# Kernel optimization log

Hardware: AMD Instinct MI355X
Metric: run time of the kernel (lower is better)

Reference implementation:

```python
import jax, jax.numpy as jnp
import numpy as np

WINDOW = 32
MALIS_LR = 1.0
MALIS_LR_POS = 1.0


def _make_node_indexes(w):
    idx = np.arange(w * w).reshape(w, w)
    h = np.stack([idx[:, :-1].ravel(), idx[:, 1:].ravel()])
    v = np.stack([idx[:-1, :].ravel(), idx[1:, :].ravel()])
    return np.concatenate([h, v], axis=1)  # [2, 2*w*(w-1)]


class _UF:
    def __init__(self, n):
        self.p = list(range(n))

    def find(self, x):
        p = self.p
        while p[x] != x:
            p[x] = p[p[x]]
            x = p[x]
        return x


def _label8(mask):
    """skimage.measure.label with full (8-)connectivity: labels>=1 inside mask, 0 outside."""
    h, w = mask.shape
    n = h * w
    uf = _UF(n)
    idx = np.arange(n).reshape(h, w)
    pairs = []
    for (a, b) in (
        (idx[:, :-1], idx[:, 1:]),      # right
        (idx[:-1, :], idx[1:, :]),      # down
        (idx[:-1, :-1], idx[1:, 1:]),   # down-right
        (idx[:-1, 1:], idx[1:, :-1]),   # down-left
    ):
        m = mask.ravel()[a.ravel()] & mask.ravel()[b.ravel()]
        pairs.append(np.stack([a.ravel()[m], b.ravel()[m]], 1))
    for a, b in np.concatenate(pairs, 0):
        ra, rb = uf.find(int(a)), uf.find(int(b))
        if ra != rb:
            uf.p[rb] = ra
    labels = np.zeros(n, dtype=np.int64)
    root_lab = {}
    nxt = 1
    flat = mask.ravel()
    for i in range(n):
        if flat[i]:
            r = uf.find(i)
            if r not in root_lab:
                root_lab[r] = nxt
                nxt += 1
            labels[i] = root_lab[r]
    return labels


def _malis_weights(seg, n1, n2, costs, pos):
    """MALIS pair counts per edge: Kruskal maximin over edges in descending cost order;
    nodes with seg label 0 (foreground in this loss) carry no labels and contribute no pairs."""
    n = seg.shape[0]
    uf = _UF(n)
    overlap = [({int(seg[i]): 1} if seg[i] != 0 else {}) for i in range(n)]
    w = np.zeros(costs.shape[0], dtype=np.int64)
    order = np.argsort(-costs, kind="stable")
    for e in order:
        ra, rb = uf.find(int(n1[e])), uf.find(int(n2[e]))
        if ra == rb:
            continue
        oa, ob = overlap[ra], overlap[rb]
        tot_a = sum(oa.values())
        npair = 0
        for l2, c2 in ob.items():
            same = oa.get(l2, 0)
            npair += c2 * (same if pos else (tot_a - same))
        w[int(e)] = npair
        uf.p[rb] = ra
        for l2, c2 in ob.items():
            oa[l2] = oa.get(l2, 0) + c2
        overlap[rb] = {}
    return w


def _connectivity_weights(y_true_np, y_pred_np, window):
    B, C, H, W = y_pred_np.shape
    ni = _make_node_indexes(window)
    n1, n2 = ni[0], ni[1]
    weights_n = np.zeros_like(y_pred_np, dtype=np.float64)
    weights_p = np.zeros_like(y_pred_np, dtype=np.float64)
    half = window * (window - 1)
    for r in range(H // window):
        for c in range(W // window):
            rs = slice(r * window, (r + 1) * window)
            cs = slice(c * window, (c + 1) * window)
            P = y_pred_np[:, :, rs, cs]
            T = y_true_np[:, :, rs, cs]
            if P.min() == 1 or P.max() == 0:
                continue
            if T.min() == 1 or T.max() == 0:
                continue
            ch = (P[:, :, :, :-1] + P[:, :, :, 1:]).reshape(B, -1)
            cv = (P[:, :, :-1, :] + P[:, :, 1:, :]).reshape(B, -1)
            costs = np.concatenate([ch, cv], 1)
            gh = (T[:, :, :, :-1] + T[:, :, :, 1:]).reshape(B, -1)
            gv = (T[:, :, :-1, :] + T[:, :, 1:, :]).reshape(B, -1)
            gt = np.concatenate([gh, gv], 1)
            costs_n = costs.copy()
            costs_p = costs.copy()
            costs_n[gt > 20] = 20
            costs_p[gt < 10] = 0
            gt = np.minimum(gt, 20)
            for i in range(B):
                seg = _label8(T[i, 0] == 0).astype(np.uint64)
                ewn = _malis_weights(seg, n1, n2, costs_n[i].astype(np.float32), 0).astype(np.float64)
                ewp = _malis_weights(seg, n1, n2, costs_p[i].astype(np.float32), 1).astype(np.float64)
                sn = ewn.sum()
                if sn > 0:
                    ewn = ewn / sn
                sp = ewp.sum()
                if sp > 0:
                    ewp = ewp / sp
                ewn[gt[i] >= 10] = 0
                ewp[gt[i] < 20] = 0
                for ew, Wacc in ((ewn, weights_n), (ewp, weights_p)):
                    wh = ew[:half].reshape(window, window - 1)
                    wv = ew[half:].reshape(window - 1, window)
                    blk = Wacc[i, 0, rs, cs]  # numpy view -> in-place scatter-add
                    blk[:, :-1] += wh
                    blk[:, 1:] += wh
                    blk[:-1, :] += wv
                    blk[1:, :] += wv
    return weights_n, weights_p


def setup_inputs() -> dict:
    key = jax.random.key(0)
    k1, k2 = jax.random.split(key)
    B, C, H, W = 2, 1, 256, 256
    # targets in {0, 20}, predictions continuous in [0, 20) -- the loss thresholds
    # (10, 20) and the (20 - y_pred)^2 term assume this scale.
    y_true = (jax.random.randint(k2, (B, C, H, W), 0, 2) * 20).astype(jnp.float32)
    y_pred = jax.random.uniform(k1, (B, C, H, W), dtype=jnp.float32) * 20.0
    return {"y_true": y_true, "y_pred": y_pred}


def reference(y_true, y_pred):
    # MALIS weights are computed on host (union-find / connected components), exactly as
    # the torch module does via skimage + malis on detached CPU numpy arrays.
    wn, wp = _connectivity_weights(np.asarray(y_true), np.asarray(y_pred), WINDOW)
    wn = jnp.asarray(wn, dtype=y_pred.dtype)
    wp = jnp.asarray(wp, dtype=y_pred.dtype)
    loss = MALIS_LR * jnp.square(y_pred) * wn + MALIS_LR_POS * jnp.square(20.0 - y_pred) * wp
    return loss.sum()
```

## Files before the change

### kernel.cpp

```cpp
#include <hip/hip_runtime.h>
#include <stdint.h>

#define NPIX 1024
#define NEDGE 1984
#define NSORT 2048
#define CROWS 64
#define CNTW (NPIX + 2)

#define WS_PART   0u
#define WS_SKIP   2048u
#define WS_NLAB   2304u
#define WS_M      2816u
#define WS_PW     4096u
#define WS_LAB    528384u
#define WS_LABD   790528u
#define WS_REC    1052672u
#define WS_MSNAP  3149824u
#define WS_SNAP   3153920u

__device__ __forceinline__ void edge_nodes(int e, int& a, int& b) {
  if (e < 992) { int r = e / 31; int c = e - r * 31; a = (r << 5) + c; b = a + 1; }
  else         { a = e - 992; b = a + 32; }
}

__device__ __forceinline__ void cinc(uint16_t* row, int root) {
  uint32_t* w = (uint32_t*)(row + (root & ~1));
  atomicAdd(w, (root & 1) ? 0x10000u : 1u);
}

__device__ __forceinline__ int uf_find(volatile uint32_t* par, int x) {
  int p = (int)par[x];
  while (p != x) {
    int gp = (int)par[p];
    par[x] = (uint32_t)gp;
    x = gp; p = (int)par[x];
  }
  return x;
}

__device__ __forceinline__ void uf_union(volatile uint32_t* par, int a, int b) {
  int ra = uf_find(par, a), rb = uf_find(par, b);
  while (ra != rb) {
    if (ra > rb) { int t2 = ra; ra = rb; rb = t2; }
    unsigned old = atomicCAS((unsigned*)(par + rb), (unsigned)rb, (unsigned)ra);
    if (old == (unsigned)rb) break;
    rb = uf_find(par, (int)old);
    ra = uf_find(par, ra);
  }
}

__global__ __launch_bounds__(256) void k1_prep(const float* __restrict__ y_true,
                                               const float* __restrict__ y_pred,
                                               char* __restrict__ ws) {
  __shared__ float    Pw[NPIX];
  __shared__ uint16_t lab[NPIX];
  __shared__ uint8_t  maskv[NPIX];
  __shared__ uint32_t lcnt[NPIX];
  __shared__ uint32_t par32[NPIX];
  __shared__ unsigned minP, maxP, minT, maxT;
  __shared__ int nl;
  const int tid = threadIdx.x, pw = blockIdx.x, bat = pw >> 6, win = pw & 63;
  const int wr = win >> 3, wc = win & 7;
  if (tid == 0) { minP = ~0u; maxP = 0u; minT = ~0u; maxT = 0u; nl = 0; }
  __syncthreads();
  {
    unsigned mnP = ~0u, mxP = 0u, mnT = ~0u, mxT = 0u;
    for (int i = tid; i < 2 * NPIX; i += 256) {
      int bb = i >> 10, p = i & (NPIX - 1);
      int r = p >> 5, c = p & 31;
      size_t g = ((size_t)(bb * 256 + wr * 32 + r)) * 256 + (size_t)(wc * 32 + c);
      float pv = y_pred[g], tv = y_true[g];
      unsigned pu = __float_as_uint(pv), tu = __float_as_uint(tv);
      mnP = min(mnP, pu); mxP = max(mxP, pu);
      mnT = min(mnT, tu); mxT = max(mxT, tu);
      if (bb == bat) {
        Pw[p] = pv; maskv[p] = (tv == 0.f) ? 1 : 0;
        par32[p] = (uint32_t)p;
        lcnt[p] = 0u;
      }
    }
    atomicMin(&minP, mnP); atomicMax(&maxP, mxP);
    atomicMin(&minT, mnT); atomicMax(&maxT, mxT);
  }
  __syncthreads();
  {
    float a = __uint_as_float(minP), b = __uint_as_float(maxP);
    float c2 = __uint_as_float(minT), d = __uint_as_float(maxT);
    int skip = (a == 1.f || b == 0.f || c2 == 1.f || d == 0.f) ? 1 : 0;
    if (tid == 0) ((uint32_t*)(ws + WS_SKIP))[win] = (uint32_t)skip;
    if (skip) return;
  }
  for (int p = tid; p < NPIX; p += 256) {
    if (!maskv[p]) continue;
    int r = p >> 5, c = p & 31;
    if (c < 31 && maskv[p + 1]) uf_union(par32, p, p + 1);
    if (r < 31) {
      if (maskv[p + 32])           uf_union(par32, p, p + 32);
      if (c < 31 && maskv[p + 33]) uf_union(par32, p, p + 33);
      if (c > 0  && maskv[p + 31]) uf_union(par32, p, p + 31);
    }
  }
  __syncthreads();
  for (int p = tid; p < NPIX; p += 256) {
    uint16_t l = 0;
    if (maskv[p]) {
      int x = p, px = (int)par32[x];
      while (px != x) { x = px; px = (int)par32[x]; }
      l = (uint16_t)(x + 1);
    }
    lab[p] = l;
  }
  __syncthreads();
  for (int p = tid; p < NPIX; p += 256)
    if (maskv[p]) atomicAdd(&lcnt[lab[p] - 1], 1u);
  __syncthreads();
  uint16_t* labDG = (uint16_t*)(ws + WS_LABD) + (size_t)pw * NPIX;
  for (int p = tid; p < NPIX; p += 256) {
    uint16_t v = 0;
    if (maskv[p] && lab[p] == (uint16_t)(p + 1) && lcnt[p] >= 2u)
      v = (uint16_t)(atomicAdd(&nl, 1) + 1);
    labDG[p] = v;
  }
  __syncthreads();
  float*    PwG  = (float*)(ws + WS_PW)  + (size_t)pw * NPIX;
  uint16_t* labG = (uint16_t*)(ws + WS_LAB) + (size_t)pw * NPIX;
  for (int p = tid; p < NPIX; p += 256) { PwG[p] = Pw[p]; labG[p] = lab[p]; }
  if (tid == 0) ((uint32_t*)(ws + WS_NLAB))[pw] = (uint32_t)nl;
}

__global__ __launch_bounds__(256) void k2ab_sortkruskal(char* __restrict__ ws) {
  __shared__ unsigned long long keys[NSORT];
  __shared__ float    Pw[NPIX];
  __shared__ uint16_t lab[NPIX];
  __shared__ uint16_t par[NPIX];
  const int tid = threadIdx.x, t = blockIdx.x;
  const int sign = t & 1, win = (t >> 1) & 63, bat = t >> 7;
  const int pw = bat * 64 + win;
  uint32_t* MG = (uint32_t*)(ws + WS_M);
  uint32_t* msW = (uint32_t*)(ws + WS_MSNAP) + t * 3;
  if (((const uint32_t*)(ws + WS_SKIP))[win]) { if (tid == 0) MG[t] = 0u; return; }
  const float*    PwG  = (const float*)(ws + WS_PW)  + (size_t)pw * NPIX;
  const uint16_t* labG = (const uint16_t*)(ws + WS_LAB) + (size_t)pw * NPIX;
  for (int p = tid; p < NPIX; p += 256) {
    Pw[p] = PwG[p]; lab[p] = labG[p]; par[p] = (uint16_t)p;
  }
  __syncthreads();
  for (int e = tid; e < NSORT; e += 256) {
    if (e < NEDGE) {
      int a, b; edge_nodes(e, a, b);
      int cls = (lab[a] ? 0 : 1) + (lab[b] ? 0 : 1);
      float cost = Pw[a] + Pw[b];
      if (sign == 0) { if (cls == 2) cost = 20.0f; }
      else           { if (cls == 0) cost = 0.0f;  }
      keys[e] = (((unsigned long long)(__float_as_uint(cost) ^ 0xFFFFFFFFu)) << 32)
                | (unsigned long long)(unsigned)e;
    } else keys[e] = ~0ull;
  }
  __syncthreads();
  {
    unsigned long long x[8];
    const int baseI = tid * 8;
    #pragma unroll
    for (int v = 0; v < 8; ++v) x[v] = keys[baseI + v];
    #pragma unroll
    for (int kk = 2; kk <= 8; kk <<= 1) {
      #pragma unroll
      for (int j = kk >> 1; j > 0; j >>= 1) {
        #pragma unroll
        for (int v = 0; v < 8; ++v) {
          int p = v ^ j;
          if (p > v) {
            bool asc = (((baseI + v) & kk) == 0);
            unsigned long long A = x[v], B = x[p];
            if ((A > B) == asc) { x[v] = B; x[p] = A; }
          }
        }
      }
    }
    #pragma unroll
    for (int v = 0; v < 8; ++v) keys[baseI + v] = x[v];
  }
  for (int k = 16; k <= NSORT; k <<= 1) {
    for (int j = k >> 1; j >= 8; j >>= 1) {
      __syncthreads();
      for (int q = tid; q < NSORT / 2; q += 256) {
        int i = ((q & ~(j - 1)) << 1) | (q & (j - 1));
        int p = i + j;
        bool asc = ((i & k) == 0);
        unsigned long long A = keys[i], B = keys[p];
        if ((A > B) == asc) { keys[i] = B; keys[p] = A; }
      }
    }
    __syncthreads();
    {
      unsigned long long x[8];
      const int baseI = tid * 8;
      const bool asc = ((baseI & k) == 0);
      #pragma unroll
      for (int v = 0; v < 8; ++v) x[v] = keys[baseI + v];
      #pragma unroll
      for (int j = 4; j > 0; j >>= 1) {
        #pragma unroll
        for (int v = 0; v < 8; ++v) {
          int p = v ^ j;
          if (p > v) {
            unsigned long long A = x[v], B = x[p];
            if ((A > B) == asc) { x[v] = B; x[p] = A; }
          }
        }
      }
      #pragma unroll
      for (int v = 0; v < 8; ++v) keys[baseI + v] = x[v];
    }
  }
  __syncthreads();
  if (tid < 64) {
    const int lane = tid;
    const uint32_t* keyLo = (const uint32_t*)keys;
    uint32_t* recG = (uint32_t*)(ws + WS_REC) + (size_t)t * NPIX;
    uint16_t* snapW = (uint16_t*)(ws + WS_SNAP) + (size_t)t * 3072;
    int mTotal = 0, nsnp = 0;
    for (int base = 0; base < NEDGE; base += 64) {
      unsigned e = keyLo[(base + lane) * 2];
      int a, b; edge_nodes((int)e, a, b);
      int xa = a, xb = b;
      for (;;) {
        int pa = par[xa], pb = par[xb];
        if (pa == xa && pb == xb) break;
        xa = pa; xb = pb;
      }
      int ra = xa, rb = xb;
      bool cand0 = (ra != rb);
      unsigned pkMe = (unsigned)ra | ((unsigned)rb << 10) | (cand0 ? (1u << 20) : 0u);
      unsigned pkPrev = (unsigned)__shfl((int)pkMe, (lane + 63) & 63, 64);
      bool cand = cand0 && !((lane > 0) && (pkPrev == pkMe));
      unsigned long long cm = __ballot(cand);
      int mb = 0;
      unsigned recP = 0u;
      while (cm) {
        int i = __ffsll((long long)cm) - 1;
        cm &= cm - 1;
        int rA = __builtin_amdgcn_readlane(ra, i);
        int rB = __builtin_amdgcn_readlane(rb, i);
        bool acc = (rA != rB);
        unsigned pk = (unsigned)i | ((unsigned)rA << 11) | ((unsigned)rB << 21);
        if (acc && lane == mb) recP = pk;
        ra = (ra == rB) ? rA : ra;
        rb = (rb == rB) ? rA : rb;
        mb += acc ? 1 : 0;
      }
      unsigned eRec = (unsigned)__shfl((int)e, (int)(recP & 63u), 64);
      if (lane < mb) {
        int rAo = (int)((recP >> 11) & 1023u);
        int rBo = (int)(recP >> 21);
        par[rBo] = (uint16_t)rAo;
        recG[mTotal + lane] = (recP & 0xFFFFF800u) | eRec;
      }
      mTotal += mb;
      if (mb > 2 && (base + 64 < NEDGE)) {
        for (int pass = 0; pass < 2; ++pass) {
          uint16_t vv[16];
          #pragma unroll
          for (int j = 0; j < 16; ++j) vv[j] = par[j * 64 + lane];
          #pragma unroll
          for (int j = 0; j < 16; ++j) vv[j] = par[vv[j]];
          #pragma unroll
          for (int j = 0; j < 16; ++j) par[j * 64 + lane] = vv[j];
        }
      }
      while (nsnp < 3 && mTotal >= 256 * (nsnp + 1)) {
        #pragma unroll
        for (int j = 0; j < 16; ++j) {
          int p = j * 64 + lane;
          int r = par[p], pr = par[r];
          while (pr != r) { r = pr; pr = par[r]; }
          snapW[nsnp * 1024 + p] = (uint16_t)r;
        }
        if (lane == 0) msW[nsnp] = (uint32_t)mTotal;
        ++nsnp;
      }
    }
    while (nsnp < 3) { if (lane == 0) msW[nsnp] = (uint32_t)mTotal; ++nsnp; }
    if (lane == 0) MG[t] = (uint32_t)mTotal;
  }
}

__global__ __launch_bounds__(256) void k2c_replay(char* __restrict__ ws) {
  __shared__ union {
    uint16_t cnt[CROWS][CNTW];
    double   red[256];
  } u;
  __shared__ float    Pw[NPIX];
  __shared__ uint16_t lab[NPIX];
  __shared__ uint16_t labD[NPIX];
  __shared__ uint32_t recW[NPIX];
  __shared__ uint32_t totp[NPIX];
  __shared__ uint32_t same[NPIX];
  __shared__ unsigned Ssum;
  const int tid = threadIdx.x, t = blockIdx.x;
  const int sign = t & 1, win = (t >> 1) & 63, bat = t >> 7;
  const int pw = bat * 64 + win;
  double* partG = (double*)(ws + WS_PART);
  if (((const uint32_t*)(ws + WS_SKIP))[win]) { if (tid == 0) partG[t] = 0.0; return; }
  const int M    = (int)((const uint32_t*)(ws + WS_M))[t];
  const int nlab = (int)((const uint32_t*)(ws + WS_NLAB))[pw];
  const uint32_t* msG = (const uint32_t*)(ws + WS_MSNAP) + t * 3;
  const uint16_t* snapG = (const uint16_t*)(ws + WS_SNAP) + (size_t)t * 3072;
  const int ms1 = (int)msG[0], ms2 = (int)msG[1], ms3 = (int)msG[2];
  if (tid == 0) Ssum = 0u;
  {
    const uint32_t* recG  = (const uint32_t*)(ws + WS_REC) + (size_t)t * NPIX;
    const float*    PwG   = (const float*)(ws + WS_PW)   + (size_t)pw * NPIX;
    const uint16_t* labG  = (const uint16_t*)(ws + WS_LAB)  + (size_t)pw * NPIX;
    const uint16_t* labDG = (const uint16_t*)(ws + WS_LABD) + (size_t)pw * NPIX;
    for (int m = tid; m < M; m += 256) { recW[m] = recG[m]; same[m] = 0u; totp[m] = 0u; }
    for (int p = tid; p < NPIX; p += 256) { Pw[p] = PwG[p]; lab[p] = labG[p]; labD[p] = labDG[p]; }
  }
  __syncthreads();

  const int wid = tid >> 6, wl = tid & 63;
  const int nRows = nlab + 1;
  for (int chb = 0; chb < nRows; chb += CROWS) {
    const int rowsHere = min(nRows - chb, CROWS);
    const int G = (rowsHere + 15) >> 4;
    const int S = (G == 1) ? 4 : ((G == 2) ? 2 : 1);
    const int g = wid / S, s = wid % S;
    const int rowLo = chb + g * 16;
    int b0, b1;
    if (S == 4)      { b0 = (s == 0) ? 0 : (s == 1 ? ms1 : (s == 2 ? ms2 : ms3));
                       b1 = (s == 0) ? ms1 : (s == 1 ? ms2 : (s == 2 ? ms3 : M)); }
    else if (S == 2) { b0 = s ? ms2 : 0; b1 = s ? M : ms2; }
    else             { b0 = 0; b1 = M; }
    const bool active = (rowLo < nRows) && (b0 < b1);

    for (int i = tid; i < (CROWS * CNTW) / 2; i += 256) ((uint32_t*)u.cnt)[i] = 0u;
    __syncthreads();
    if (active) {
      const int rowHi = min(rowLo + 16, nRows);
      for (int p = wl; p < NPIX; p += 64) {
        uint16_t l = lab[p];
        if (!l) continue;
        int root = (s == 0) ? p : (int)snapG[(s - 1) * 1024 + p];
        int d = labD[l - 1];
        if (d) { int dl = d - 1; if (dl >= rowLo && dl < rowHi) cinc(u.cnt[wid * 16 + (dl - rowLo)], root); }
        if (nlab >= rowLo && nlab < rowHi) cinc(u.cnt[wid * 16 + (nlab - rowLo)], root);
      }
    }
    __syncthreads();
    if (active && wl < 16) {
      int logical = rowLo + wl;
      if (logical < nRows) {
        const bool isP = (logical == nlab);
        uint16_t* C = u.cnt[wid * 16 + wl];
        int lastRa = -1; unsigned lastVal = 0;
        int pfr = -1; unsigned pfv = 0;
        unsigned w = recW[b0];
        int ra = (int)((w >> 11) & 1023u), rb = (int)(w >> 21);
        unsigned caL = C[ra], cbL = C[rb];
        for (int m = b0; m < b1; ++m) {
          int mn = (m + 1 < b1) ? m + 1 : m;
          unsigned wN = recW[mn];
          int raN = (int)((wN >> 11) & 1023u), rbN = (int)(wN >> 21);
          unsigned caN = C[raN], cbN = C[rbN];
          unsigned ca = (ra == lastRa) ? lastVal : ((ra == pfr) ? pfv : caL);
          unsigned cb = (rb == lastRa) ? lastVal : ((rb == pfr) ? pfv : cbL);
          int npfr = -1; unsigned npfv = 0;
          if (ra != lastRa) {
            if (lastRa >= 0) { C[lastRa] = (uint16_t)lastVal; npfr = lastRa; npfv = lastVal; }
            lastRa = ra; lastVal = ca;
          }
          if (cb) {
            if (isP) totp[m] = lastVal * cb;
            else if (lastVal) atomicAdd(&same[m], lastVal * cb);
            lastVal += cb;
          }
          pfr = npfr; pfv = npfv;
          ra = raN; rb = rbN; caL = caN; cbL = cbN;
        }
      }
    }
    __syncthreads();
  }

  unsigned mys = 0u;
  for (int m = tid; m < M; m += 256)
    mys += sign ? same[m] : (totp[m] - same[m]);
  atomicAdd(&Ssum, mys);
  __syncthreads();
  const unsigned S = Ssum;

  double part = 0.0;
  if (S > 0u) {
    for (int m = tid; m < M; m += 256) {
      unsigned np = sign ? same[m] : (totp[m] - same[m]);
      if (np == 0u) continue;
      int e = (int)(recW[m] & 2047u);
      int a, b; edge_nodes(e, a, b);
      int cls = (lab[a] ? 0 : 1) + (lab[b] ? 0 : 1);
      bool keep = sign ? (cls != 0)
                       : (cls == 0);
      if (!keep) continue;
      double fa, fb;
      if (sign) {
        double da = 20.0 - (double)Pw[a], db = 20.0 - (double)Pw[b];
        fa = da * da; fb = db * db;
      } else {
        fa = (double)Pw[a] * (double)Pw[a];
        fb = (double)Pw[b] * (double)Pw[b];
      }
      part += (double)np * (fa + fb);
    }
  }
  u.red[tid] = part;
  __syncthreads();
  for (int st = 128; st > 0; st >>= 1) {
    if (tid < st) u.red[tid] += u.red[tid + st];
    __syncthreads();
  }
  if (tid == 0) partG[t] = (S > 0u) ? (u.red[0] / (double)S) : 0.0;
}

__global__ __launch_bounds__(256) void final_reduce(
    const double* __restrict__ part, float* __restrict__ out)
{
  __shared__ double r[256];
  int tdx = threadIdx.x;
  r[tdx] = part[tdx];
  __syncthreads();
  for (int st = 128; st > 0; st >>= 1) {
    if (tdx < st) r[tdx] += r[tdx + st];
    __syncthreads();
  }
  if (tdx == 0) out[0] = (float)r[0];
}

extern "C" void kernel_launch(void* const* d_in, const int* in_sizes, int n_in,
                              void* d_out, int out_size, void* d_ws, size_t ws_size,
                              hipStream_t stream) {
  const float* y_true = (const float*)d_in[0];
  const float* y_pred = (const float*)d_in[1];
  char* ws = (char*)d_ws;
  k1_prep<<<128, 256, 0, stream>>>(y_true, y_pred, ws);
  k2ab_sortkruskal<<<256, 256, 0, stream>>>(ws);
  k2c_replay<<<256, 256, 0, stream>>>(ws);
  final_reduce<<<1, 256, 0, stream>>>((const double*)(ws + WS_PART), (float*)d_out);
}
```

Measured before the change: 285.9 us.

## Fuse prep, sort-Kruskal and replay kernels into one shared-memory megakernel

Merges the three per-window kernels into a single kernel with 256 blocks. Each block recomputes the connected-component labelling for its window and keeps labels, Kruskal records and snapshots in shared memory instead of passing them through global workspace. This removes two kernel launches and the workspace round trips. In exchange the labelling work is done twice (once per sign), and the larger unioned shared-memory footprint may lower occupancy.

```diff
diff --git a/kernel.cpp b/kernel.cpp
--- a/kernel.cpp
+++ b/kernel.cpp
@@ -7,17 +7,6 @@
 #define CROWS 64
 #define CNTW (NPIX + 2)
 
-#define WS_PART   0u
-#define WS_SKIP   2048u
-#define WS_NLAB   2304u
-#define WS_M      2816u
-#define WS_PW     4096u
-#define WS_LAB    528384u
-#define WS_LABD   790528u
-#define WS_REC    1052672u
-#define WS_MSNAP  3149824u
-#define WS_SNAP   3153920u
-
 __device__ __forceinline__ void edge_nodes(int e, int& a, int& b) {
   if (e < 992) { int r = e / 31; int c = e - r * 31; a = (r << 5) + c; b = a + 1; }
   else         { a = e - 992; b = a + 32; }
@@ -28,41 +17,42 @@
   atomicAdd(w, (root & 1) ? 0x10000u : 1u);
 }
 
-__device__ __forceinline__ int uf_find(volatile uint32_t* par, int x) {
-  int p = (int)par[x];
-  while (p != x) {
-    int gp = (int)par[p];
-    par[x] = (uint32_t)gp;
-    x = gp; p = (int)par[x];
-  }
-  return x;
-}
-
-__device__ __forceinline__ void uf_union(volatile uint32_t* par, int a, int b) {
-  int ra = uf_find(par, a), rb = uf_find(par, b);
-  while (ra != rb) {
-    if (ra > rb) { int t2 = ra; ra = rb; rb = t2; }
-    unsigned old = atomicCAS((unsigned*)(par + rb), (unsigned)rb, (unsigned)ra);
-    if (old == (unsigned)rb) break;
-    rb = uf_find(par, (int)old);
-    ra = uf_find(par, ra);
-  }
-}
-
-__global__ __launch_bounds__(256) void k1_prep(const float* __restrict__ y_true,
-                                               const float* __restrict__ y_pred,
-                                               char* __restrict__ ws) {
-  __shared__ float    Pw[NPIX];
-  __shared__ uint16_t lab[NPIX];
-  __shared__ uint8_t  maskv[NPIX];
-  __shared__ uint32_t lcnt[NPIX];
-  __shared__ uint32_t par32[NPIX];
-  __shared__ unsigned minP, maxP, minT, maxT;
-  __shared__ int nl;
-  const int tid = threadIdx.x, pw = blockIdx.x, bat = pw >> 6, win = pw & 63;
+struct SMem {
+  union {
+    uint16_t cnt[CROWS][CNTW];
+    struct {
+      unsigned long long keys[NSORT];
+      uint16_t par[NPIX];
+    } sk;
+    struct {
+      uint32_t par32[NPIX];
+      uint32_t lcnt[NPIX];
+      uint8_t  maskv[NPIX];
+    } pp;
+    double red[256];
+  } u;
+  float    Pw[NPIX];
+  uint16_t lab[NPIX];
+  uint16_t labD[NPIX];
+  uint32_t recW[NPIX];
+  uint32_t totp[NPIX];
+  uint32_t same[NPIX];
+  uint16_t snapL[3][NPIX];
+  unsigned minP, maxP, minT, maxT, Ssum;
+  int nl, Msh, ms[3];
+};
+
+__global__ __launch_bounds__(256) void mega(const float* __restrict__ y_true,
+                                            const float* __restrict__ y_pred,
+                                            double* __restrict__ partG) {
+  __shared__ SMem s;
+  const int tid = threadIdx.x, t = blockIdx.x;
+  const int sign = t & 1, win = (t >> 1) & 63, bat = t >> 7;
   const int wr = win >> 3, wc = win & 7;
-  if (tid == 0) { minP = ~0u; maxP = 0u; minT = ~0u; maxT = 0u; nl = 0; }
-  __syncthreads();
+  if (tid == 0) { s.minP = ~0u; s.maxP = 0u; s.minT = ~0u; s.maxT = 0u;
+                  s.nl = 0; s.Msh = 0; s.Ssum = 0u; }
+  __syncthreads();
+
   {
     unsigned mnP = ~0u, mxP = 0u, mnT = ~0u, mxT = 0u;
     for (int i = tid; i < 2 * NPIX; i += 256) {
@@ -74,94 +64,99 @@
       mnP = min(mnP, pu); mxP = max(mxP, pu);
       mnT = min(mnT, tu); mxT = max(mxT, tu);
       if (bb == bat) {
-        Pw[p] = pv; maskv[p] = (tv == 0.f) ? 1 : 0;
-        par32[p] = (uint32_t)p;
-        lcnt[p] = 0u;
-      }
-    }
-    atomicMin(&minP, mnP); atomicMax(&maxP, mxP);
-    atomicMin(&minT, mnT); atomicMax(&maxT, mxT);
+        s.Pw[p] = pv; s.u.pp.maskv[p] = (tv == 0.f) ? 1 : 0;
+        s.u.pp.par32[p] = (uint32_t)p;
+        s.u.pp.lcnt[p] = 0u;
+      }
+    }
+    atomicMin(&s.minP, mnP); atomicMax(&s.maxP, mxP);
+    atomicMin(&s.minT, mnT); atomicMax(&s.maxT, mxT);
   }
   __syncthreads();
   {
-    float a = __uint_as_float(minP), b = __uint_as_float(maxP);
-    float c2 = __uint_as_float(minT), d = __uint_as_float(maxT);
-    int skip = (a == 1.f || b == 0.f || c2 == 1.f || d == 0.f) ? 1 : 0;
-    if (tid == 0) ((uint32_t*)(ws + WS_SKIP))[win] = (uint32_t)skip;
-    if (skip) return;
-  }
-  for (int p = tid; p < NPIX; p += 256) {
-    if (!maskv[p]) continue;
-    int r = p >> 5, c = p & 31;
-    if (c < 31 && maskv[p + 1]) uf_union(par32, p, p + 1);
-    if (r < 31) {
-      if (maskv[p + 32])           uf_union(par32, p, p + 32);
-      if (c < 31 && maskv[p + 33]) uf_union(par32, p, p + 33);
-      if (c > 0  && maskv[p + 31]) uf_union(par32, p, p + 31);
+    float a = __uint_as_float(s.minP), b = __uint_as_float(s.maxP);
+    float c2 = __uint_as_float(s.minT), d = __uint_as_float(s.maxT);
+    if (a == 1.f || b == 0.f || c2 == 1.f || d == 0.f) {
+      if (tid == 0) partG[t] = 0.0;
+      return;
+    }
+  }
+  {
+    volatile uint32_t* par32 = (volatile uint32_t*)s.u.pp.par32;
+    uint8_t* maskv = s.u.pp.maskv;
+    for (int p = tid; p < NPIX; p += 256) {
+      if (!maskv[p]) continue;
+      int r = p >> 5, c = p & 31;
+      int nb[4]; int nn = 0;
+      if (c < 31 && maskv[p + 1]) nb[nn++] = p + 1;
+      if (r < 31) {
+        if (maskv[p + 32])           nb[nn++] = p + 32;
+        if (c < 31 && maskv[p + 33]) nb[nn++] = p + 33;
+        if (c > 0  && maskv[p + 31]) nb[nn++] = p + 31;
+      }
+      for (int q = 0; q < nn; ++q) {
+        int x = p, px = (int)par32[x];
+        while (px != x) { int gp = (int)par32[px]; par32[x] = (uint32_t)gp; x = gp; px = (int)par32[x]; }
+        int ra = x;
+        x = nb[q]; px = (int)par32[x];
+        while (px != x) { int gp = (int)par32[px]; par32[x] = (uint32_t)gp; x = gp; px = (int)par32[x]; }
+        int rb = x;
+        while (ra != rb) {
+          if (ra > rb) { int t2 = ra; ra = rb; rb = t2; }
+          unsigned old = atomicCAS((unsigned*)(par32 + rb), (unsigned)rb, (unsigned)ra);
+          if (old == (unsigned)rb) break;
+          x = (int)old; px = (int)par32[x];
+          while (px != x) { x = px; px = (int)par32[x]; }
+          rb = x;
+          x = ra; px = (int)par32[x];
+          while (px != x) { x = px; px = (int)par32[x]; }
+          ra = x;
+        }
+      }
     }
   }
   __syncthreads();
   for (int p = tid; p < NPIX; p += 256) {
     uint16_t l = 0;
-    if (maskv[p]) {
-      int x = p, px = (int)par32[x];
-      while (px != x) { x = px; px = (int)par32[x]; }
+    if (s.u.pp.maskv[p]) {
+      int x = p, px = (int)s.u.pp.par32[x];
+      while (px != x) { x = px; px = (int)s.u.pp.par32[x]; }
       l = (uint16_t)(x + 1);
     }
-    lab[p] = l;
+    s.lab[p] = l;
   }
   __syncthreads();
   for (int p = tid; p < NPIX; p += 256)
-    if (maskv[p]) atomicAdd(&lcnt[lab[p] - 1], 1u);
-  __syncthreads();
-  uint16_t* labDG = (uint16_t*)(ws + WS_LABD) + (size_t)pw * NPIX;
+    if (s.lab[p]) atomicAdd(&s.u.pp.lcnt[s.lab[p] - 1], 1u);
+  __syncthreads();
   for (int p = tid; p < NPIX; p += 256) {
     uint16_t v = 0;
-    if (maskv[p] && lab[p] == (uint16_t)(p + 1) && lcnt[p] >= 2u)
-      v = (uint16_t)(atomicAdd(&nl, 1) + 1);
-    labDG[p] = v;
-  }
-  __syncthreads();
-  float*    PwG  = (float*)(ws + WS_PW)  + (size_t)pw * NPIX;
-  uint16_t* labG = (uint16_t*)(ws + WS_LAB) + (size_t)pw * NPIX;
-  for (int p = tid; p < NPIX; p += 256) { PwG[p] = Pw[p]; labG[p] = lab[p]; }
-  if (tid == 0) ((uint32_t*)(ws + WS_NLAB))[pw] = (uint32_t)nl;
-}
-
-__global__ __launch_bounds__(256) void k2ab_sortkruskal(char* __restrict__ ws) {
-  __shared__ unsigned long long keys[NSORT];
-  __shared__ float    Pw[NPIX];
-  __shared__ uint16_t lab[NPIX];
-  __shared__ uint16_t par[NPIX];
-  const int tid = threadIdx.x, t = blockIdx.x;
-  const int sign = t & 1, win = (t >> 1) & 63, bat = t >> 7;
-  const int pw = bat * 64 + win;
-  uint32_t* MG = (uint32_t*)(ws + WS_M);
-  uint32_t* msW = (uint32_t*)(ws + WS_MSNAP) + t * 3;
-  if (((const uint32_t*)(ws + WS_SKIP))[win]) { if (tid == 0) MG[t] = 0u; return; }
-  const float*    PwG  = (const float*)(ws + WS_PW)  + (size_t)pw * NPIX;
-  const uint16_t* labG = (const uint16_t*)(ws + WS_LAB) + (size_t)pw * NPIX;
-  for (int p = tid; p < NPIX; p += 256) {
-    Pw[p] = PwG[p]; lab[p] = labG[p]; par[p] = (uint16_t)p;
-  }
-  __syncthreads();
+    if (s.lab[p] && s.lab[p] == (uint16_t)(p + 1) && s.u.pp.lcnt[p] >= 2u)
+      v = (uint16_t)(atomicAdd(&s.nl, 1) + 1);
+    s.labD[p] = v;
+  }
+  for (int p = tid; p < NPIX; p += 256) { s.same[p] = 0u; s.totp[p] = 0u; }
+  __syncthreads();
+  const int nlab = s.nl;
+
   for (int e = tid; e < NSORT; e += 256) {
     if (e < NEDGE) {
       int a, b; edge_nodes(e, a, b);
-      int cls = (lab[a] ? 0 : 1) + (lab[b] ? 0 : 1);
-      float cost = Pw[a] + Pw[b];
+      int cls = (s.lab[a] ? 0 : 1) + (s.lab[b] ? 0 : 1);
+      float cost = s.Pw[a] + s.Pw[b];
       if (sign == 0) { if (cls == 2) cost = 20.0f; }
       else           { if (cls == 0) cost = 0.0f;  }
-      keys[e] = (((unsigned long long)(__float_as_uint(cost) ^ 0xFFFFFFFFu)) << 32)
-                | (unsigned long long)(unsigned)e;
-    } else keys[e] = ~0ull;
-  }
+      s.u.sk.keys[e] = (((unsigned long long)(__float_as_uint(cost) ^ 0xFFFFFFFFu)) << 32)
+                       | (unsigned long long)(unsigned)e;
+    } else s.u.sk.keys[e] = ~0ull;
+  }
+  for (int p = tid; p < NPIX; p += 256) s.u.sk.par[p] = (uint16_t)p;
   __syncthreads();
   {
     unsigned long long x[8];
     const int baseI = tid * 8;
     #pragma unroll
-    for (int v = 0; v < 8; ++v) x[v] = keys[baseI + v];
+    for (int v = 0; v < 8; ++v) x[v] = s.u.sk.keys[baseI + v];
     #pragma unroll
     for (int kk = 2; kk <= 8; kk <<= 1) {
       #pragma unroll
@@ -178,7 +173,7 @@
       }
     }
     #pragma unroll
-    for (int v = 0; v < 8; ++v) keys[baseI + v] = x[v];
+    for (int v = 0; v < 8; ++v) s.u.sk.keys[baseI + v] = x[v];
   }
   for (int k = 16; k <= NSORT; k <<= 1) {
     for (int j = k >> 1; j >= 8; j >>= 1) {
@@ -187,8 +182,8 @@
         int i = ((q & ~(j - 1)) << 1) | (q & (j - 1));
         int p = i + j;
         bool asc = ((i & k) == 0);
-        unsigned long long A = keys[i], B = keys[p];
-        if ((A > B) == asc) { keys[i] = B; keys[p] = A; }
+        unsigned long long A = s.u.sk.keys[i], B = s.u.sk.keys[p];
+        if ((A > B) == asc) { s.u.sk.keys[i] = B; s.u.sk.keys[p] = A; }
       }
     }
     __syncthreads();
@@ -197,7 +192,7 @@
       const int baseI = tid * 8;
       const bool asc = ((baseI & k) == 0);
       #pragma unroll
-      for (int v = 0; v < 8; ++v) x[v] = keys[baseI + v];
+      for (int v = 0; v < 8; ++v) x[v] = s.u.sk.keys[baseI + v];
       #pragma unroll
       for (int j = 4; j > 0; j >>= 1) {
         #pragma unroll
@@ -210,15 +205,15 @@
         }
       }
       #pragma unroll
-      for (int v = 0; v < 8; ++v) keys[baseI + v] = x[v];
-    }
-  }
-  __syncthreads();
+      for (int v = 0; v < 8; ++v) s.u.sk.keys[baseI + v] = x[v];
+    }
+  }
+  __syncthreads();
+
   if (tid < 64) {
     const int lane = tid;
-    const uint32_t* keyLo = (const uint32_t*)keys;
-    uint32_t* recG = (uint32_t*)(ws + WS_REC) + (size_t)t * NPIX;
-    uint16_t* snapW = (uint16_t*)(ws + WS_SNAP) + (size_t)t * 3072;
+    const uint32_t* keyLo = (const uint32_t*)s.u.sk.keys;
+    uint16_t* par = s.u.sk.par;
     int mTotal = 0, nsnp = 0;
     for (int base = 0; base < NEDGE; base += 64) {
       unsigned e = keyLo[(base + lane) * 2];
@@ -254,7 +249,7 @@
         int rAo = (int)((recP >> 11) & 1023u);
         int rBo = (int)(recP >> 21);
         par[rBo] = (uint16_t)rAo;
-        recG[mTotal + lane] = (recP & 0xFFFFF800u) | eRec;
+        s.recW[mTotal + lane] = (recP & 0xFFFFF800u) | eRec;
       }
       mTotal += mb;
       if (mb > 2 && (base + 64 < NEDGE)) {
@@ -274,49 +269,18 @@
           int p = j * 64 + lane;
           int r = par[p], pr = par[r];
           while (pr != r) { r = pr; pr = par[r]; }
-          snapW[nsnp * 1024 + p] = (uint16_t)r;
-        }
-        if (lane == 0) msW[nsnp] = (uint32_t)mTotal;
+          s.snapL[nsnp][p] = (uint16_t)r;
+        }
+        if (lane == 0) s.ms[nsnp] = mTotal;
         ++nsnp;
       }
     }
-    while (nsnp < 3) { if (lane == 0) msW[nsnp] = (uint32_t)mTotal; ++nsnp; }
-    if (lane == 0) MG[t] = (uint32_t)mTotal;
-  }
-}
-
-__global__ __launch_bounds__(256) void k2c_replay(char* __restrict__ ws) {
-  __shared__ union {
-    uint16_t cnt[CROWS][CNTW];
-    double   red[256];
-  } u;
-  __shared__ float    Pw[NPIX];
-  __shared__ uint16_t lab[NPIX];
-  __shared__ uint16_t labD[NPIX];
-  __shared__ uint32_t recW[NPIX];
-  __shared__ uint32_t totp[NPIX];
-  __shared__ uint32_t same[NPIX];
-  __shared__ unsigned Ssum;
-  const int tid = threadIdx.x, t = blockIdx.x;
-  const int sign = t & 1, win = (t >> 1) & 63, bat = t >> 7;
-  const int pw = bat * 64 + win;
-  double* partG = (double*)(ws + WS_PART);
-  if (((const uint32_t*)(ws + WS_SKIP))[win]) { if (tid == 0) partG[t] = 0.0; return; }
-  const int M    = (int)((const uint32_t*)(ws + WS_M))[t];
-  const int nlab = (int)((const uint32_t*)(ws + WS_NLAB))[pw];
-  const uint32_t* msG = (const uint32_t*)(ws + WS_MSNAP) + t * 3;
-  const uint16_t* snapG = (const uint16_t*)(ws + WS_SNAP) + (size_t)t * 3072;
-  const int ms1 = (int)msG[0], ms2 = (int)msG[1], ms3 = (int)msG[2];
-  if (tid == 0) Ssum = 0u;
-  {
-    const uint32_t* recG  = (const uint32_t*)(ws + WS_REC) + (size_t)t * NPIX;
-    const float*    PwG   = (const float*)(ws + WS_PW)   + (size_t)pw * NPIX;
-    const uint16_t* labG  = (const uint16_t*)(ws + WS_LAB)  + (size_t)pw * NPIX;
-    const uint16_t* labDG = (const uint16_t*)(ws + WS_LABD) + (size_t)pw * NPIX;
-    for (int m = tid; m < M; m += 256) { recW[m] = recG[m]; same[m] = 0u; totp[m] = 0u; }
-    for (int p = tid; p < NPIX; p += 256) { Pw[p] = PwG[p]; lab[p] = labG[p]; labD[p] = labDG[p]; }
-  }
-  __syncthreads();
+    while (nsnp < 3) { if (lane == 0) s.ms[nsnp] = mTotal; ++nsnp; }
+    if (lane == 0) s.Msh = mTotal;
+  }
+  __syncthreads();
+  const int M = s.Msh;
+  const int ms1 = s.ms[0], ms2 = s.ms[1], ms3 = s.ms[2];
 
   const int wid = tid >> 6, wl = tid & 63;
   const int nRows = nlab + 1;
@@ -324,26 +288,26 @@
     const int rowsHere = min(nRows - chb, CROWS);
     const int G = (rowsHere + 15) >> 4;
     const int S = (G == 1) ? 4 : ((G == 2) ? 2 : 1);
-    const int g = wid / S, s = wid % S;
+    const int g = wid / S, sseg = wid % S;
     const int rowLo = chb + g * 16;
     int b0, b1;
-    if (S == 4)      { b0 = (s == 0) ? 0 : (s == 1 ? ms1 : (s == 2 ? ms2 : ms3));
-                       b1 = (s == 0) ? ms1 : (s == 1 ? ms2 : (s == 2 ? ms3 : M)); }
-    else if (S == 2) { b0 = s ? ms2 : 0; b1 = s ? M : ms2; }
+    if (S == 4)      { b0 = (sseg == 0) ? 0 : (sseg == 1 ? ms1 : (sseg == 2 ? ms2 : ms3));
+                       b1 = (sseg == 0) ? ms1 : (sseg == 1 ? ms2 : (sseg == 2 ? ms3 : M)); }
+    else if (S == 2) { b0 = sseg ? ms2 : 0; b1 = sseg ? M : ms2; }
     else             { b0 = 0; b1 = M; }
     const bool active = (rowLo < nRows) && (b0 < b1);
 
-    for (int i = tid; i < (CROWS * CNTW) / 2; i += 256) ((uint32_t*)u.cnt)[i] = 0u;
+    for (int i = tid; i < (CROWS * CNTW) / 2; i += 256) ((uint32_t*)s.u.cnt)[i] = 0u;
     __syncthreads();
     if (active) {
       const int rowHi = min(rowLo + 16, nRows);
       for (int p = wl; p < NPIX; p += 64) {
-        uint16_t l = lab[p];
+        uint16_t l = s.lab[p];
         if (!l) continue;
-        int root = (s == 0) ? p : (int)snapG[(s - 1) * 1024 + p];
-        int d = labD[l - 1];
-        if (d) { int dl = d - 1; if (dl >= rowLo && dl < rowHi) cinc(u.cnt[wid * 16 + (dl - rowLo)], root); }
-        if (nlab >= rowLo && nlab < rowHi) cinc(u.cnt[wid * 16 + (nlab - rowLo)], root);
+        int root = (sseg == 0) ? p : (int)s.snapL[sseg - 1][p];
+        int d = s.labD[l - 1];
+        if (d) { int dl = d - 1; if (dl >= rowLo && dl < rowHi) cinc(s.u.cnt[wid * 16 + (dl - rowLo)], root); }
+        if (nlab >= rowLo && nlab < rowHi) cinc(s.u.cnt[wid * 16 + (nlab - rowLo)], root);
       }
     }
     __syncthreads();
@@ -351,15 +315,15 @@
       int logical = rowLo + wl;
       if (logical < nRows) {
         const bool isP = (logical == nlab);
-        uint16_t* C = u.cnt[wid * 16 + wl];
+        uint16_t* C = s.u.cnt[wid * 16 + wl];
         int lastRa = -1; unsigned lastVal = 0;
         int pfr = -1; unsigned pfv = 0;
-        unsigned w = recW[b0];
+        unsigned w = s.recW[b0];
         int ra = (int)((w >> 11) & 1023u), rb = (int)(w >> 21);
         unsigned caL = C[ra], cbL = C[rb];
         for (int m = b0; m < b1; ++m) {
           int mn = (m + 1 < b1) ? m + 1 : m;
-          unsigned wN = recW[mn];
+          unsigned wN = s.recW[mn];
           int raN = (int)((wN >> 11) & 1023u), rbN = (int)(wN >> 21);
           unsigned caN = C[raN], cbN = C[rbN];
           unsigned ca = (ra == lastRa) ? lastVal : ((ra == pfr) ? pfv : caL);
@@ -370,8 +334,8 @@
             lastRa = ra; lastVal = ca;
           }
           if (cb) {
-            if (isP) totp[m] = lastVal * cb;
-            else if (lastVal) atomicAdd(&same[m], lastVal * cb);
+            if (isP) s.totp[m] = lastVal * cb;
+            else if (lastVal) atomicAdd(&s.same[m], lastVal * cb);
             lastVal += cb;
           }
           pfr = npfr; pfv = npfv;
@@ -384,40 +348,40 @@
 
   unsigned mys = 0u;
   for (int m = tid; m < M; m += 256)
-    mys += sign ? same[m] : (totp[m] - same[m]);
-  atomicAdd(&Ssum, mys);
-  __syncthreads();
-  const unsigned S = Ssum;
+    mys += sign ? s.same[m] : (s.totp[m] - s.same[m]);
+  atomicAdd(&s.Ssum, mys);
+  __syncthreads();
+  const unsigned S = s.Ssum;
 
   double part = 0.0;
   if (S > 0u) {
     for (int m = tid; m < M; m += 256) {
-      unsigned np = sign ? same[m] : (totp[m] - same[m]);
+      unsigned np = sign ? s.same[m] : (s.totp[m] - s.same[m]);
       if (np == 0u) continue;
-      int e = (int)(recW[m] & 2047u);
+      int e = (int)(s.recW[m] & 2047u);
       int a, b; edge_nodes(e, a, b);
-      int cls = (lab[a] ? 0 : 1) + (lab[b] ? 0 : 1);
+      int cls = (s.lab[a] ? 0 : 1) + (s.lab[b] ? 0 : 1);
       bool keep = sign ? (cls != 0)
                        : (cls == 0);
       if (!keep) continue;
       double fa, fb;
       if (sign) {
-        double da = 20.0 - (double)Pw[a], db = 20.0 - (double)Pw[b];
+        double da = 20.0 - (double)s.Pw[a], db = 20.0 - (double)s.Pw[b];
         fa = da * da; fb = db * db;
       } else {
-        fa = (double)Pw[a] * (double)Pw[a];
-        fb = (double)Pw[b] * (double)Pw[b];
+        fa = (double)s.Pw[a] * (double)s.Pw[a];
+        fb = (double)s.Pw[b] * (double)s.Pw[b];
       }
       part += (double)np * (fa + fb);
     }
   }
-  u.red[tid] = part;
+  s.u.red[tid] = part;
   __syncthreads();
   for (int st = 128; st > 0; st >>= 1) {
-    if (tid < st) u.red[tid] += u.red[tid + st];
-    __syncthreads();
-  }
-  if (tid == 0) partG[t] = (S > 0u) ? (u.red[0] / (double)S) : 0.0;
+    if (tid < st) s.u.red[tid] += s.u.red[tid + st];
+    __syncthreads();
+  }
+  if (tid == 0) partG[t] = (S > 0u) ? (s.u.red[0] / (double)S) : 0.0;
 }
 
 __global__ __launch_bounds__(256) void final_reduce(
@@ -439,9 +403,7 @@
                               hipStream_t stream) {
   const float* y_true = (const float*)d_in[0];
   const float* y_pred = (const float*)d_in[1];
-  char* ws = (char*)d_ws;
-  k1_prep<<<128, 256, 0, stream>>>(y_true, y_pred, ws);
-  k2ab_sortkruskal<<<256, 256, 0, stream>>>(ws);
-  k2c_replay<<<256, 256, 0, stream>>>(ws);
-  final_reduce<<<1, 256, 0, stream>>>((const double*)(ws + WS_PART), (float*)d_out);
+  double* wsd = (double*)d_ws;
+  mega<<<256, 256, 0, stream>>>(y_true, y_pred, wsd);
+  final_reduce<<<1, 256, 0, stream>>>(wsd, (float*)d_out);
 }
```

Measured after the change: 272.6 us. 4.7% less time.
